# Performance work log

Hardware: AMD Instinct MI355X
Metric: run time of the kernel (lower is better)

The kernel has to match this reference:

```python
import jax, jax.numpy as jnp
import numpy as np

N = 50000   # nodes
E = 400000  # edges
R = 35      # num_relations
B = 12      # num_bases
C = 128     # hidden_conv_dim (heads=1)
T = 4       # node types: load, gen, load_gen, ext
HL = 38     # hidden_lin_dim
OUT = 2


def setup_inputs() -> dict:
    key = jax.random.key(0)
    ks = jax.random.split(key, 24)
    s = 0.1  # param scale
    inp = {
        'x': jax.random.normal(ks[0], (N, 2), jnp.float32),
        'edge_index': jax.random.randint(ks[1], (2, E), 0, N, jnp.int32),
        'edge_type': jax.random.randint(ks[2], (E,), 0, R, jnp.int32),
        'edge_attr': jax.random.normal(ks[3], (E, 2), jnp.float32),
        'node_type': jax.random.randint(ks[4], (N,), 0, T, jnp.int32),
        'basis': jax.random.normal(ks[5], (B, 2, C), jnp.float32) * s,
        'att_rel': jax.random.normal(ks[6], (R, B), jnp.float32) * s,
        'q_att': jax.random.normal(ks[7], (C, 1), jnp.float32) * s,
        'k_att': jax.random.normal(ks[8], (C, 1), jnp.float32) * s,
        'e_att': jax.random.normal(ks[9], (C, 1), jnp.float32) * s,
        'lin_edge_W': jax.random.normal(ks[10], (2, C), jnp.float32) * s,
        'conv_bias': jax.random.normal(ks[11], (C,), jnp.float32) * s,
        'lin0_W': jax.random.normal(ks[12], (T, C, HL), jnp.float32) * s,
        'lin0_b': jax.random.normal(ks[13], (T, HL), jnp.float32) * s,
        'lin1_W': jax.random.normal(ks[14], (T, HL, HL), jnp.float32) * s,
        'lin1_b': jax.random.normal(ks[15], (T, HL), jnp.float32) * s,
        'lin2_W': jax.random.normal(ks[16], (T, HL, HL), jnp.float32) * s,
        'lin2_b': jax.random.normal(ks[17], (T, HL), jnp.float32) * s,
        'fin_W': jax.random.normal(ks[18], (T, HL, OUT), jnp.float32) * s,
        'fin_b': jax.random.normal(ks[19], (T, OUT), jnp.float32) * s,
    }
    return inp


def _segment_softmax(alpha, dst, n):
    # PyG softmax: max is detached, eps=1e-16 on the denominator
    amax = jax.lax.stop_gradient(jax.ops.segment_max(alpha, dst, num_segments=n))
    ex = jnp.exp(alpha - amax[dst])
    den = jax.ops.segment_sum(ex, dst, num_segments=n) + 1e-16
    return ex / den[dst]


def _per_type_linear(xv, W, b, t):
    # apply node-type-specific Linear: [N,d] x [T,d,h] -> pick row type
    y = jnp.einsum('nd,tdh->nth', xv, W)              # [N,T,h]
    y = jnp.take_along_axis(y, t[:, None, None], axis=1)[:, 0]
    return y + b[t]


def reference(x, edge_index, edge_type, edge_attr, node_type,
              basis, att_rel, q_att, k_att, e_att, lin_edge_W, conv_bias,
              lin0_W, lin0_b, lin1_W, lin1_b, lin2_W, lin2_b, fin_W, fin_b):
    n = x.shape[0]
    src, dst = edge_index[0], edge_index[1]
    # RGATConv with basis decomposition: per-relation weight [R, in=2, C]
    w = jnp.einsum('rb,bio->rio', att_rel, basis)
    w_e = w[edge_type]                                 # [E,2,C] edge gather
    out_i = jnp.einsum('ei,eic->ec', x[dst], w_e)      # [E,C]
    out_j = jnp.einsum('ei,eic->ec', x[src], w_e)      # [E,C]
    ke = (edge_attr @ lin_edge_W) @ e_att              # [E,1]
    alpha = out_i @ q_att + out_j @ k_att + ke         # additive self-attention
    alpha = jax.nn.leaky_relu(alpha, 0.2)
    alpha = _segment_softmax(alpha, dst, n)            # across-relation segment softmax
    msg = alpha * out_j                                # heads=1 -> [E,C]
    agg = jax.ops.segment_sum(msg, dst, num_segments=n) + conv_bias
    h = jax.nn.leaky_relu(agg, 0.2)                    # forward activation (dropout: eval)
    t = node_type
    h = _per_type_linear(jax.nn.relu(h), lin0_W, lin0_b, t)
    h = _per_type_linear(jax.nn.relu(h), lin1_W, lin1_b, t)
    h = _per_type_linear(jax.nn.relu(h), lin2_W, lin2_b, t)
    out = _per_type_linear(h, fin_W, fin_b, t)         # [N,2]
    # load nodes (type 0): second output passes through abs
    load_out = jnp.concatenate([out[:, :1], jnp.abs(out[:, 1:2])], axis=1)
    return jnp.where((t == 0)[:, None], load_out, out)
```

## Files before the change

kernel.cpp:

```cpp
#include <hip/hip_runtime.h>
#include <math.h>

#define N_NODES 50000
#define N_EDGES 400000
#define R_REL   35
#define B_BASES 12
#define C_DIM   128
#define HL_DIM  38
#define RI2     70
#define NP      50304
#define NB_HIST 196
#define NBUCK   786
#define EPB     2048
#define CAP     704

#define OFF_WT     0
#define OFF_WQ     8960
#define OFF_WK     9030
#define OFF_LE     9100
#define OFF_META   9104
#define OFF_HBLK   9120
#define OFF_PERM   10688
#define OFF_INV    60688
#define OFF_ECUR   110992
#define OFF_EREC   111780

#define CH    0
#define ST    3584
#define HH    0
#define Y0T   0
#define W1S   3264
#define W2S   4784
#define Y1T   6304
#define Y2T   0
#define W0Q   8344
#define SM_DINV 9624
#define SM_FW   9688
#define SM_FB   9764
#define LDS_FLOATS 9766

__global__ __launch_bounds__(256) void k_init(const int* __restrict__ node_type,
                                              const float* __restrict__ basis,
                                              const float* __restrict__ att_rel,
                                              const float* __restrict__ q_att,
                                              const float* __restrict__ k_att,
                                              const float* __restrict__ e_att,
                                              const float* __restrict__ lin_edge_W,
                                              float* __restrict__ ws) {
    int b = blockIdx.x, tid = threadIdx.x;
    if (b < NB_HIST) {
        __shared__ int lh[4];
        if (tid < 4) lh[tid] = 0;
        __syncthreads();
        int i = b * 256 + tid;
        if (i < N_NODES) atomicAdd(&lh[node_type[i]], 1);
        __syncthreads();
        if (tid < 4) ((int*)(ws + OFF_HBLK))[b * 4 + tid] = lh[tid];
    } else if (b < NB_HIST + 35) {
        int idx = (b - NB_HIST) * 256 + tid;
        if (idx < RI2 * C_DIM) {
            int c  = idx & (C_DIM - 1);
            int ri = idx >> 7;
            int r = ri >> 1, ii = ri & 1;
            float acc = 0.f;
            #pragma unroll
            for (int bb = 0; bb < B_BASES; ++bb)
                acc += att_rel[r * B_BASES + bb] * basis[(bb * 2 + ii) * C_DIM + c];
            ws[OFF_WT + idx] = acc;
        }
    } else if (b == NB_HIST + 35) {
        for (int i = tid; i < NBUCK; i += 256) ((int*)(ws + OFF_ECUR))[i] = 0;
    } else {
        int lane = tid & 63, wv = tid >> 6;
        int u = (b - (NB_HIST + 36)) * 4 + wv;
        if (u < 2 * RI2) {
            int ri = (u < RI2) ? u : (u - RI2);
            int r = ri >> 1, ii = ri & 1;
            const float* av = att_rel + r * B_BASES;
            const float* bs = basis + ii * C_DIM;
            float w1 = 0.f, w2 = 0.f;
            #pragma unroll
            for (int bb = 0; bb < B_BASES; ++bb) {
                float a = av[bb];
                w1 += a * bs[bb * 2 * C_DIM + lane];
                w2 += a * bs[bb * 2 * C_DIM + 64 + lane];
            }
            const float* qk = (u < RI2) ? q_att : k_att;
            float s = w1 * qk[lane] + w2 * qk[64 + lane];
            #pragma unroll
            for (int off = 32; off; off >>= 1) s += __shfl_xor(s, off, 64);
            if (lane == 0) ws[((u < RI2) ? OFF_WQ : OFF_WK) + ri] = s;
        } else if (u < 2 * RI2 + 2) {
            int j = u - 2 * RI2;
            const float* er = lin_edge_W + j * C_DIM;
            float s = er[lane] * e_att[lane] + er[64 + lane] * e_att[64 + lane];
            #pragma unroll
            for (int off = 32; off; off >>= 1) s += __shfl_xor(s, off, 64);
            if (lane == 0) ws[OFF_LE + j] = s;
        }
    }
}

__global__ __launch_bounds__(256) void k_perm(const int* __restrict__ node_type,
                                              float* __restrict__ ws) {
    __shared__ int lh[NB_HIST * 4];
    __shared__ int pre[4], tot[4], basel[4];
    __shared__ int wcnt[4][4];
    int tid = threadIdx.x;
    int lane = tid & 63, wv = tid >> 6;
    const int* hblk = (const int*)(ws + OFF_HBLK);
    for (int i = tid; i < NB_HIST * 4; i += 256) lh[i] = hblk[i];
    __syncthreads();
    if (tid < 4) {
        int run = 0, mypre = 0;
        for (int bb = 0; bb < NB_HIST; ++bb) {
            if (bb == (int)blockIdx.x) mypre = run;
            run += lh[bb * 4 + tid];
        }
        pre[tid] = mypre;
        tot[tid] = run;
    }
    __syncthreads();
    if (tid == 0) {
        int t0 = tot[0], t1 = tot[1], t2 = tot[2];
        int b1 = ((t0 + 63) >> 6) << 6;
        int b2 = b1 + (((t1 + 63) >> 6) << 6);
        int b3 = b2 + (((t2 + 63) >> 6) << 6);
        basel[0] = 0; basel[1] = b1; basel[2] = b2; basel[3] = b3;
        if (blockIdx.x == 0) {
            int* meta = (int*)(ws + OFF_META);
            meta[0] = t0; meta[1] = t1; meta[2] = t2; meta[3] = tot[3];
            meta[4] = 0;  meta[5] = b1; meta[6] = b2; meta[7] = b3;
        }
    }
    __syncthreads();
    int n = blockIdx.x * 256 + tid;
    bool active = n < N_NODES;
    int ty = active ? node_type[n] : -1;
    int myrank = 0;
    #pragma unroll
    for (int t = 0; t < 4; ++t) {
        unsigned long long m = __ballot(ty == t);
        if (lane == 0) wcnt[wv][t] = __popcll(m);
        if (ty == t) myrank = __popcll(m & ((1ULL << lane) - 1ULL));
    }
    __syncthreads();
    if (active) {
        int prew = 0;
        for (int w2 = 0; w2 < wv; ++w2) prew += wcnt[w2][ty];
        int p = basel[ty] + pre[ty] + prew + myrank;
        ((int*)(ws + OFF_PERM))[n] = p;
        ((int*)(ws + OFF_INV))[p] = n;
    }
}

__global__ __launch_bounds__(256) void k_escatter(const float* __restrict__ x,
                                                  const int* __restrict__ edge_index,
                                                  const int* __restrict__ edge_type,
                                                  const float* __restrict__ edge_attr,
                                                  float* __restrict__ ws) {
    __shared__ int hist[NBUCK];
    __shared__ int sbase[NBUCK];
    __shared__ float swq[RI2], swk[RI2], sle[2];
    int tid = threadIdx.x;
    for (int i = tid; i < NBUCK; i += 256) hist[i] = 0;
    if (tid < RI2) { swq[tid] = ws[OFF_WQ + tid]; swk[tid] = ws[OFF_WK + tid]; }
    if (tid < 2) sle[tid] = ws[OFF_LE + tid];
    __syncthreads();

    const int* perm = (const int*)(ws + OFF_PERM);
    int base = blockIdx.x * EPB;
    int   rb[8], rm[8];
    float rex[8], rsx[8], rsy[8];
    #pragma unroll
    for (int k = 0; k < 8; ++k) {
        int e = base + k * 256 + tid;
        rb[k] = -1;
        if (e < N_EDGES) {
            int src = edge_index[e];
            int dst = edge_index[N_EDGES + e];
            int r   = edge_type[e];
            int p   = perm[dst];
            float2 ea = *(const float2*)(edge_attr + 2 * e);
            float2 xs = *(const float2*)(x + 2 * src);
            float2 xd = *(const float2*)(x + 2 * dst);
            float alpha = xd.x * swq[2 * r] + xd.y * swq[2 * r + 1]
                        + xs.x * swk[2 * r] + xs.y * swk[2 * r + 1]
                        + ea.x * sle[0]     + ea.y * sle[1];
            alpha = alpha > 0.f ? alpha : 0.2f * alpha;
            float ex = __expf(alpha);
            rb[k]  = p >> 6;
            rm[k]  = (r << 6) | (p & 63);
            rex[k] = ex;
            rsx[k] = ex * xs.x;
            rsy[k] = ex * xs.y;
            atomicAdd(&hist[rb[k]], 1);
        }
    }
    __syncthreads();
    int* gcur = (int*)(ws + OFF_ECUR);
    for (int i = tid; i < NBUCK; i += 256) {
        int c = hist[i];
        sbase[i] = (c > 0) ? atomicAdd(&gcur[i], c) : 0;
    }
    __syncthreads();
    float4* rec = (float4*)(ws + OFF_EREC);
    #pragma unroll
    for (int k = 0; k < 8; ++k) {
        if (rb[k] >= 0) {
            int slot = atomicAdd(&sbase[rb[k]], 1);
            rec[(size_t)rb[k] * CAP + slot] =
                make_float4(__int_as_float(rm[k]), rex[k], rsx[k], rsy[k]);
        }
    }
}

__global__ __launch_bounds__(256) void k_node(
        const float* __restrict__ ws, const float* __restrict__ conv_bias,
        const float* __restrict__ lin0_W, const float* __restrict__ lin0_b,
        const float* __restrict__ lin1_W, const float* __restrict__ lin1_b,
        const float* __restrict__ lin2_W, const float* __restrict__ lin2_b,
        const float* __restrict__ fin_W,  const float* __restrict__ fin_b,
        float* __restrict__ out) {
    __shared__ float L[LDS_FLOATS];
    int tid  = threadIdx.x;
    int lane = tid & 63;
    int wv   = tid >> 6;
    int p0   = blockIdx.x * 64;

    const int* meta = (const int*)(ws + OFF_META);
    int b1 = meta[5], b2 = meta[6], b3 = meta[7];
    int t  = (p0 >= b1) + (p0 >= b2) + (p0 >= b3);
    int bp = meta[4 + t];
    int cnt = meta[t];

    for (int i = tid; i < RI2 * 68; i += 256) L[ST + i] = 0.f;
    if (tid < 64) L[SM_DINV + tid] = 0.f;
    if (tid >= 64 && tid < 142) {
        int i = tid - 64;
        if (i < 76) L[SM_FW + i] = fin_W[t * 76 + i];
        else        L[SM_FB + i - 76] = fin_b[t * 2 + i - 76];
    }
    const float* wT_g = ws + OFF_WT;
    for (int i4 = tid; i4 < 448; i4 += 256) {
        float4 v = ((const float4*)wT_g)[i4];
        *(float4*)&L[CH + i4 * 4] = v;
    }
    __syncthreads();

    {
        int ecnt = ((const int*)(ws + OFF_ECUR))[blockIdx.x];
        const float4* rec = (const float4*)(ws + OFF_EREC) + (size_t)blockIdx.x * CAP;
        for (int i = tid; i < ecnt; i += 256) {
            float4 v = rec[i];
            int m = __float_as_int(v.x);
            int n = m & 63, r = m >> 6;
            atomicAdd(&L[ST + (2 * r) * 68 + n],     v.z);
            atomicAdd(&L[ST + (2 * r + 1) * 68 + n], v.w);
            atomicAdd(&L[SM_DINV + n],               v.y);
        }
    }
    __syncthreads();
    if (tid < 64) L[SM_DINV + tid] = 1.0f / (L[SM_DINV + tid] + 1e-16f);

    int ng = lane & 15, cg_ = lane >> 4;
    int c0 = wv * 32 + cg_ * 8;
    float acc[32];
    #pragma unroll
    for (int i = 0; i < 32; ++i) acc[i] = 0.f;
    int cur = 0;
    for (int q = 0; q < 5; ++q) {
        float4 pf0, pf1;
        if (q < 4) {
            const float4* src = (const float4*)(wT_g + (q + 1) * 1792);
            pf0 = src[tid];
            if (tid < 192) pf1 = src[tid + 256];
        }
        const float* wb = &L[CH + cur * 1792];
        #pragma unroll
        for (int kk = 0; kk < 14; ++kk) {
            float4 a4 = *(const float4*)&L[ST + (q * 14 + kk) * 68 + ng * 4];
            float4 wa = *(const float4*)&wb[kk * 128 + c0];
            float4 wc = *(const float4*)&wb[kk * 128 + c0 + 4];
            float a_[4] = {a4.x, a4.y, a4.z, a4.w};
            float w_[8] = {wa.x, wa.y, wa.z, wa.w, wc.x, wc.y, wc.z, wc.w};
            #pragma unroll
            for (int ni = 0; ni < 4; ++ni)
                #pragma unroll
                for (int ci = 0; ci < 8; ++ci)
                    acc[ni * 8 + ci] += a_[ni] * w_[ci];
        }
        if (q < 4) {
            float* dstb = &L[CH + (cur ^ 1) * 1792];
            *(float4*)&dstb[tid * 4] = pf0;
            if (tid < 192) *(float4*)&dstb[(tid + 256) * 4] = pf1;
        }
        cur ^= 1;
        __syncthreads();
    }

    {
        float4 dv = *(const float4*)&L[SM_DINV + ng * 4];
        float d_[4] = {dv.x, dv.y, dv.z, dv.w};
        #pragma unroll
        for (int ci = 0; ci < 8; ++ci) {
            float cb = conv_bias[c0 + ci];
            float4 hv;
            float h0 = acc[0 * 8 + ci] * d_[0] + cb;
            float h1 = acc[1 * 8 + ci] * d_[1] + cb;
            float h2 = acc[2 * 8 + ci] * d_[2] + cb;
            float h3 = acc[3 * 8 + ci] * d_[3] + cb;
            hv.x = h0 > 0.f ? h0 : 0.f;
            hv.y = h1 > 0.f ? h1 : 0.f;
            hv.z = h2 > 0.f ? h2 : 0.f;
            hv.w = h3 > 0.f ? h3 : 0.f;
            *(float4*)&L[HH + (c0 + ci) * 64 + ng * 4] = hv;
        }
    }
    __syncthreads();

    const float* W0g = lin0_W + t * C_DIM * HL_DIM;
    int jg = lane >> 4;
    int j0 = wv * 16 + jg * 4;
    float acc2[16];
    #pragma unroll
    for (int i = 0; i < 16; ++i) acc2[i] = 0.f;
    for (int q = 0; q < 4; ++q) {
        for (int i = tid; i < 1216; i += 256) {
            int cc = i / 38, j = i - cc * 38;
            L[W0Q + cc * 40 + j] = W0g[q * 1216 + i];
        }
        __syncthreads();
        if (wv < 3) {
            #pragma unroll 4
            for (int kk = 0; kk < 32; ++kk) {
                int c = q * 32 + kk;
                float4 a4 = *(const float4*)&L[HH + c * 64 + ng * 4];
                float4 w4 = *(const float4*)&L[W0Q + kk * 40 + j0];
                float a_[4] = {a4.x, a4.y, a4.z, a4.w};
                float w_[4] = {w4.x, w4.y, w4.z, w4.w};
                #pragma unroll
                for (int ni = 0; ni < 4; ++ni)
                    #pragma unroll
                    for (int ji = 0; ji < 4; ++ji)
                        acc2[ni * 4 + ji] += a_[ni] * w_[ji];
            }
        }
        __syncthreads();
    }
    if (wv < 3) {
        #pragma unroll
        for (int ji = 0; ji < 4; ++ji) {
            int j = j0 + ji;
            float b = (j < HL_DIM) ? lin0_b[t * HL_DIM + j] : 0.f;
            float4 yv;
            float y0 = acc2[0 * 4 + ji] + b;
            float y1 = acc2[1 * 4 + ji] + b;
            float y2 = acc2[2 * 4 + ji] + b;
            float y3 = acc2[3 * 4 + ji] + b;
            yv.x = y0 > 0.f ? y0 : 0.f;
            yv.y = y1 > 0.f ? y1 : 0.f;
            yv.z = y2 > 0.f ? y2 : 0.f;
            yv.w = y3 > 0.f ? y3 : 0.f;
            *(float4*)&L[Y0T + j * 68 + ng * 4] = yv;
        }
    }
    {
        const float* W1g = lin1_W + t * HL_DIM * HL_DIM;
        const float* W2g = lin2_W + t * HL_DIM * HL_DIM;
        for (int i = tid; i < 1444; i += 256) {
            int cc = i / 38, j = i - cc * 38;
            L[W1S + cc * 40 + j] = W1g[i];
            L[W2S + cc * 40 + j] = W2g[i];
        }
    }
    __syncthreads();

    float acc3[16];
    #pragma unroll
    for (int i = 0; i < 16; ++i) acc3[i] = 0.f;
    if (wv < 3) {
        #pragma unroll 2
        for (int kk = 0; kk < HL_DIM; ++kk) {
            float4 a4 = *(const float4*)&L[Y0T + kk * 68 + ng * 4];
            float4 w4 = *(const float4*)&L[W1S + kk * 40 + j0];
            float a_[4] = {a4.x, a4.y, a4.z, a4.w};
            float w_[4] = {w4.x, w4.y, w4.z, w4.w};
            #pragma unroll
            for (int ni = 0; ni < 4; ++ni)
                #pragma unroll
                for (int ji = 0; ji < 4; ++ji)
                    acc3[ni * 4 + ji] += a_[ni] * w_[ji];
        }
        #pragma unroll
        for (int ji = 0; ji < 4; ++ji) {
            int j = j0 + ji;
            float b = (j < HL_DIM) ? lin1_b[t * HL_DIM + j] : 0.f;
            float4 yv;
            float y0 = acc3[0 * 4 + ji] + b;
            float y1 = acc3[1 * 4 + ji] + b;
            float y2 = acc3[2 * 4 + ji] + b;
            float y3 = acc3[3 * 4 + ji] + b;
            yv.x = y0 > 0.f ? y0 : 0.f;
            yv.y = y1 > 0.f ? y1 : 0.f;
            yv.z = y2 > 0.f ? y2 : 0.f;
            yv.w = y3 > 0.f ? y3 : 0.f;
            *(float4*)&L[Y1T + j * 68 + ng * 4] = yv;
        }
    }
    __syncthreads();

    if (wv < 3) {
        float acc4[16];
        #pragma unroll
        for (int i = 0; i < 16; ++i) acc4[i] = 0.f;
        #pragma unroll 2
        for (int kk = 0; kk < HL_DIM; ++kk) {
            float4 a4 = *(const float4*)&L[Y1T + kk * 68 + ng * 4];
            float4 w4 = *(const float4*)&L[W2S + kk * 40 + j0];
            float a_[4] = {a4.x, a4.y, a4.z, a4.w};
            float w_[4] = {w4.x, w4.y, w4.z, w4.w};
            #pragma unroll
            for (int ni = 0; ni < 4; ++ni)
                #pragma unroll
                for (int ji = 0; ji < 4; ++ji)
                    acc4[ni * 4 + ji] += a_[ni] * w_[ji];
        }
        #pragma unroll
        for (int ji = 0; ji < 4; ++ji) {
            int j = j0 + ji;
            float b = (j < HL_DIM) ? lin2_b[t * HL_DIM + j] : 0.f;
            float4 yv;
            yv.x = acc4[0 * 4 + ji] + b;
            yv.y = acc4[1 * 4 + ji] + b;
            yv.z = acc4[2 * 4 + ji] + b;
            yv.w = acc4[3 * 4 + ji] + b;
            *(float4*)&L[Y2T + j * 68 + ng * 4] = yv;
        }
    }
    __syncthreads();

    if (tid < 64) {
        int p = p0 + tid;
        bool valid = (p - bp) < cnt;
        float o0 = L[SM_FB], o1 = L[SM_FB + 1];
        for (int jj = 0; jj < HL_DIM; ++jj) {
            float v = L[Y2T + jj * 68 + tid];
            float2 f = *(const float2*)&L[SM_FW + jj * 2];
            o0 += v * f.x;
            o1 += v * f.y;
        }
        if (t == 0) o1 = fabsf(o1);
        if (valid) {
            int orig = ((const int*)(ws + OFF_INV))[p];
            ((float2*)out)[orig] = make_float2(o0, o1);
        }
    }
}

extern "C" void kernel_launch(void* const* d_in, const int* in_sizes, int n_in,
                              void* d_out, int out_size, void* d_ws, size_t ws_size,
                              hipStream_t stream) {
    const float* x          = (const float*)d_in[0];
    const int*   edge_index = (const int*)  d_in[1];
    const int*   edge_type  = (const int*)  d_in[2];
    const float* edge_attr  = (const float*)d_in[3];
    const int*   node_type  = (const int*)  d_in[4];
    const float* basis      = (const float*)d_in[5];
    const float* att_rel    = (const float*)d_in[6];
    const float* q_att      = (const float*)d_in[7];
    const float* k_att      = (const float*)d_in[8];
    const float* e_att      = (const float*)d_in[9];
    const float* lin_edge_W = (const float*)d_in[10];
    const float* conv_bias  = (const float*)d_in[11];
    const float* lin0_W     = (const float*)d_in[12];
    const float* lin0_b     = (const float*)d_in[13];
    const float* lin1_W     = (const float*)d_in[14];
    const float* lin1_b     = (const float*)d_in[15];
    const float* lin2_W     = (const float*)d_in[16];
    const float* lin2_b     = (const float*)d_in[17];
    const float* fin_W      = (const float*)d_in[18];
    const float* fin_b      = (const float*)d_in[19];

    float* ws  = (float*)d_ws;
    float* out = (float*)d_out;

    k_init    <<<NB_HIST + 35 + 1 + 36, 256, 0, stream>>>(node_type, basis, att_rel,
                                                          q_att, k_att, e_att, lin_edge_W, ws);
    k_perm    <<<NB_HIST, 256, 0, stream>>>(node_type, ws);
    k_escatter<<<NB_HIST, 256, 0, stream>>>(x, edge_index, edge_type, edge_attr, ws);
    k_node    <<<NBUCK, 256, 0, stream>>>(ws, conv_bias,
                                          lin0_W, lin0_b, lin1_W, lin1_b,
                                          lin2_W, lin2_b, fin_W, fin_b, out);
}
```

Measured before the change: 176.1 us.

## Stage full relation and lin0 weights in LDS upfront, remove chunked double-buffering

The fused node kernel now loads the whole 70x128 transformed basis weight matrix and the full per-type lin0 weight matrix into LDS at the start. Previously it streamed them in chunks, double-buffering the basis weights and loading lin0 in four quarters. This removes several block-wide barriers and the chunk loops, and moves the lin1/lin2 weight staging earlier. The cost is LDS per block growing from about 39 KB to about 76 KB, which may cut how many blocks fit per CU and so lower occupancy.

```diff
diff --git a/kernel.cpp b/kernel.cpp
--- a/kernel.cpp
+++ b/kernel.cpp
@@ -25,19 +25,19 @@
 #define OFF_ECUR   110992
 #define OFF_EREC   111780
 
-#define CH    0
-#define ST    3584
+#define ST    0
+#define WT    4760
 #define HH    0
 #define Y0T   0
-#define W1S   3264
-#define W2S   4784
-#define Y1T   6304
+#define Y1T   3264
 #define Y2T   0
-#define W0Q   8344
-#define SM_DINV 9624
-#define SM_FW   9688
-#define SM_FB   9764
-#define LDS_FLOATS 9766
+#define W1S   8192
+#define W2S   9720
+#define W0F   13720
+#define SM_DINV 18888
+#define SM_FW   18952
+#define SM_FB   19028
+#define LDS_FLOATS 19030
 
 __global__ __launch_bounds__(256) void k_init(const int* __restrict__ node_type,
                                               const float* __restrict__ basis,
@@ -242,9 +242,14 @@
         else        L[SM_FB + i - 76] = fin_b[t * 2 + i - 76];
     }
     const float* wT_g = ws + OFF_WT;
-    for (int i4 = tid; i4 < 448; i4 += 256) {
+    for (int i4 = tid; i4 < 2240; i4 += 256) {
         float4 v = ((const float4*)wT_g)[i4];
-        *(float4*)&L[CH + i4 * 4] = v;
+        *(float4*)&L[WT + i4 * 4] = v;
+    }
+    const float* W0g = lin0_W + t * C_DIM * HL_DIM;
+    for (int i = tid; i < C_DIM * HL_DIM; i += 256) {
+        int cc = i / 38, j = i - cc * 38;
+        L[W0F + cc * 40 + j] = W0g[i];
     }
     __syncthreads();
 
@@ -268,36 +273,20 @@
     float acc[32];
     #pragma unroll
     for (int i = 0; i < 32; ++i) acc[i] = 0.f;
-    int cur = 0;
-    for (int q = 0; q < 5; ++q) {
-        float4 pf0, pf1;
-        if (q < 4) {
-            const float4* src = (const float4*)(wT_g + (q + 1) * 1792);
-            pf0 = src[tid];
-            if (tid < 192) pf1 = src[tid + 256];
-        }
-        const float* wb = &L[CH + cur * 1792];
-        #pragma unroll
-        for (int kk = 0; kk < 14; ++kk) {
-            float4 a4 = *(const float4*)&L[ST + (q * 14 + kk) * 68 + ng * 4];
-            float4 wa = *(const float4*)&wb[kk * 128 + c0];
-            float4 wc = *(const float4*)&wb[kk * 128 + c0 + 4];
-            float a_[4] = {a4.x, a4.y, a4.z, a4.w};
-            float w_[8] = {wa.x, wa.y, wa.z, wa.w, wc.x, wc.y, wc.z, wc.w};
-            #pragma unroll
-            for (int ni = 0; ni < 4; ++ni)
-                #pragma unroll
-                for (int ci = 0; ci < 8; ++ci)
-                    acc[ni * 8 + ci] += a_[ni] * w_[ci];
-        }
-        if (q < 4) {
-            float* dstb = &L[CH + (cur ^ 1) * 1792];
-            *(float4*)&dstb[tid * 4] = pf0;
-            if (tid < 192) *(float4*)&dstb[(tid + 256) * 4] = pf1;
-        }
-        cur ^= 1;
-        __syncthreads();
-    }
+    #pragma unroll 5
+    for (int kk = 0; kk < RI2; ++kk) {
+        float4 a4 = *(const float4*)&L[ST + kk * 68 + ng * 4];
+        float4 wa = *(const float4*)&L[WT + kk * 128 + c0];
+        float4 wc = *(const float4*)&L[WT + kk * 128 + c0 + 4];
+        float a_[4] = {a4.x, a4.y, a4.z, a4.w};
+        float w_[8] = {wa.x, wa.y, wa.z, wa.w, wc.x, wc.y, wc.z, wc.w};
+        #pragma unroll
+        for (int ni = 0; ni < 4; ++ni)
+            #pragma unroll
+            for (int ci = 0; ci < 8; ++ci)
+                acc[ni * 8 + ci] += a_[ni] * w_[ci];
+    }
+    __syncthreads();
 
     {
         float4 dv = *(const float4*)&L[SM_DINV + ng * 4];
@@ -317,37 +306,38 @@
             *(float4*)&L[HH + (c0 + ci) * 64 + ng * 4] = hv;
         }
     }
-    __syncthreads();
-
-    const float* W0g = lin0_W + t * C_DIM * HL_DIM;
+    {
+        const float* W1g = lin1_W + t * HL_DIM * HL_DIM;
+        const float* W2g = lin2_W + t * HL_DIM * HL_DIM;
+        for (int i = tid; i < HL_DIM * HL_DIM; i += 256) {
+            int cc = i / 38, j = i - cc * 38;
+            L[W1S + cc * 40 + j] = W1g[i];
+            L[W2S + cc * 40 + j] = W2g[i];
+        }
+    }
+    __syncthreads();
+
     int jg = lane >> 4;
     int j0 = wv * 16 + jg * 4;
     float acc2[16];
     #pragma unroll
     for (int i = 0; i < 16; ++i) acc2[i] = 0.f;
-    for (int q = 0; q < 4; ++q) {
-        for (int i = tid; i < 1216; i += 256) {
-            int cc = i / 38, j = i - cc * 38;
-            L[W0Q + cc * 40 + j] = W0g[q * 1216 + i];
-        }
-        __syncthreads();
-        if (wv < 3) {
-            #pragma unroll 4
-            for (int kk = 0; kk < 32; ++kk) {
-                int c = q * 32 + kk;
-                float4 a4 = *(const float4*)&L[HH + c * 64 + ng * 4];
-                float4 w4 = *(const float4*)&L[W0Q + kk * 40 + j0];
-                float a_[4] = {a4.x, a4.y, a4.z, a4.w};
-                float w_[4] = {w4.x, w4.y, w4.z, w4.w};
+    if (wv < 3) {
+        #pragma unroll 4
+        for (int kk = 0; kk < C_DIM; ++kk) {
+            float4 a4 = *(const float4*)&L[HH + kk * 64 + ng * 4];
+            float4 w4 = *(const float4*)&L[W0F + kk * 40 + j0];
+            float a_[4] = {a4.x, a4.y, a4.z, a4.w};
+            float w_[4] = {w4.x, w4.y, w4.z, w4.w};
+            #pragma unroll
+            for (int ni = 0; ni < 4; ++ni)
                 #pragma unroll
-                for (int ni = 0; ni < 4; ++ni)
-                    #pragma unroll
-                    for (int ji = 0; ji < 4; ++ji)
-                        acc2[ni * 4 + ji] += a_[ni] * w_[ji];
-            }
-        }
-        __syncthreads();
-    }
+                for (int ji = 0; ji < 4; ++ji)
+                    acc2[ni * 4 + ji] += a_[ni] * w_[ji];
+        }
+    }
+    __syncthreads();
+
     if (wv < 3) {
         #pragma unroll
         for (int ji = 0; ji < 4; ++ji) {
@@ -365,21 +355,12 @@
             *(float4*)&L[Y0T + j * 68 + ng * 4] = yv;
         }
     }
-    {
-        const float* W1g = lin1_W + t * HL_DIM * HL_DIM;
-        const float* W2g = lin2_W + t * HL_DIM * HL_DIM;
-        for (int i = tid; i < 1444; i += 256) {
-            int cc = i / 38, j = i - cc * 38;
-            L[W1S + cc * 40 + j] = W1g[i];
-            L[W2S + cc * 40 + j] = W2g[i];
-        }
-    }
-    __syncthreads();
-
-    float acc3[16];
-    #pragma unroll
-    for (int i = 0; i < 16; ++i) acc3[i] = 0.f;
+    __syncthreads();
+
     if (wv < 3) {
+        float acc3[16];
+        #pragma unroll
+        for (int i = 0; i < 16; ++i) acc3[i] = 0.f;
         #pragma unroll 2
         for (int kk = 0; kk < HL_DIM; ++kk) {
             float4 a4 = *(const float4*)&L[Y0T + kk * 68 + ng * 4];
```

After: 172.9 us. Within noise of the previous version (-1.8%).
